# Kernel tuning notes

Measured on AMD Instinct MI355X. Metric: run time of the kernel, lower is better.

## Reference

```python
import jax, jax.numpy as jnp
import numpy as np

B, L, TOPK, NUM_RBF, NUM_POS, MAX_REL, CH = 4, 1024, 30, 16, 16, 32, 128
EDGE_IN = NUM_POS + NUM_RBF * 25 + 18  # 434
NODE_IN = 22


def _normalize(x, axis=-1):
    n = jnp.linalg.norm(x, axis=axis, keepdims=True)
    return jnp.where(n > 0, x / jnp.where(n > 0, n, 1.0), 0.0)


def layer_norm(x, g, b, eps=1e-5):
    mu = jnp.mean(x, axis=-1, keepdims=True)
    var = jnp.var(x, axis=-1, keepdims=True)
    return (x - mu) / jnp.sqrt(var + eps) * g + b


def gather_nodes_d(nodes, idx):
    # nodes [B,M,C], idx [B,N,K] -> [B,N,K,C]
    Bn, N, K = idx.shape
    out = jnp.take_along_axis(nodes, idx.reshape(Bn, N * K, 1), axis=1)
    return out.reshape(Bn, N, K, nodes.shape[-1])


def gather_edges(edges, idx):
    # edges [B,N,N,C], idx [B,N,K] -> [B,N,K,C]
    return jnp.take_along_axis(edges, idx[..., None], axis=2)


def cal_dihedral(Xf, eps=1e-7):
    U = _normalize(Xf[:, 1:, :] - Xf[:, :-1, :])
    u_0, u_1, u_2 = U[:, :-2], U[:, 1:-1], U[:, 2:]
    n_0 = _normalize(jnp.cross(u_0, u_1))
    n_1 = _normalize(jnp.cross(u_1, u_2))
    cosD = jnp.clip(jnp.sum(n_0 * n_1, -1), -1 + eps, 1 - eps)
    v = _normalize(jnp.cross(n_0, n_1))
    return jnp.sign(jnp.sum(-v * u_1, -1)) * jnp.arccos(cosD)


def _dihedrals(X, eps=1e-7):
    Bn, N = X.shape[0], X.shape[1]
    Xf = X[:, :, :3, :].reshape(Bn, 3 * N, 3)
    D = jnp.pad(cal_dihedral(Xf), ((0, 0), (1, 2))).reshape(Bn, N, 3)
    dihedral_feats = jnp.concatenate([jnp.cos(D), jnp.sin(D)], -1)
    U = _normalize(Xf[:, 1:, :] - Xf[:, :-1, :])
    cosA = jnp.clip(jnp.sum(U[:, :-2] * U[:, 1:-1], -1), -1 + eps, 1 - eps)
    A = jnp.pad(jnp.arccos(cosA), ((0, 0), (1, 2))).reshape(Bn, N, 3)
    angle_feats = jnp.concatenate([jnp.cos(A), jnp.sin(A)], -1)
    return jnp.concatenate([dihedral_feats, angle_feats], -1)  # [B,N,12]


def _quaternions(R):
    diag = jnp.diagonal(R, axis1=-2, axis2=-1)
    Rxx, Ryy, Rzz = diag[..., 0], diag[..., 1], diag[..., 2]
    mags = 0.5 * jnp.sqrt(jnp.abs(1.0 + jnp.stack([Rxx - Ryy - Rzz, -Rxx + Ryy - Rzz, -Rxx - Ryy + Rzz], -1)))
    signs = jnp.sign(jnp.stack([R[..., 2, 1] - R[..., 1, 2], R[..., 0, 2] - R[..., 2, 0], R[..., 1, 0] - R[..., 0, 1]], -1))
    w = jnp.sqrt(jax.nn.relu(1.0 + jnp.sum(diag, -1, keepdims=True))) / 2.0
    return _normalize(jnp.concatenate([signs * mags, w], -1))


def _orientations_coarse_gl_tuple(X, E_idx):
    V = X  # [B,N,4,3]
    Bn, N = X.shape[0], X.shape[1]
    Xf = X[:, :, :3, :].reshape(Bn, 3 * N, 3)
    U = _normalize(Xf[:, 1:, :] - Xf[:, :-1, :])
    u_0, u_1 = U[:, :-2], U[:, 1:-1]
    n_0 = _normalize(jnp.cross(u_0, u_1))[:, ::3]  # [B,N-1,3]
    b_1 = _normalize(u_0 - u_1)[:, ::3]
    Xa = Xf[:, ::3]  # N-atom coords [B,N,3]
    Q = jnp.stack([b_1, n_0, jnp.cross(b_1, n_0)], 2).reshape(Bn, N - 1, 9)
    Q = jnp.pad(Q, ((0, 0), (0, 1), (0, 0)))  # [B,N,9]
    Qm = Q.reshape(Bn, N, 3, 3)
    Q_neighbors = gather_nodes_d(Q, E_idx).reshape(Bn, N, -1, 3, 3)
    X_nb = gather_nodes_d(V[:, :, 1, :], E_idx)
    N_nb = gather_nodes_d(V[:, :, 0, :], E_idx)
    C_nb = gather_nodes_d(V[:, :, 2, :], E_idx)
    O_nb = gather_nodes_d(V[:, :, 3, :], E_idx)
    dXn = jnp.stack([X_nb, N_nb, C_nb, O_nb], 3) - Xa[:, :, None, None, :]  # [B,N,K,4,3]
    dU = jnp.einsum('bnij,bnkaj->bnkai', Qm, dXn)
    Kn = E_idx.shape[-1]
    E_direct = _normalize(dU).reshape(Bn, N, Kn, 12)
    R = jnp.einsum('bnji,bnkjl->bnkil', Qm, Q_neighbors)
    q = _quaternions(R)  # [B,N,K,4]
    dX_inner = V[:, :, jnp.array([0, 2, 3]), :] - Xa[:, :, None, :]
    V_direct = _normalize(jnp.einsum('bnij,bnaj->bnai', Qm, dX_inner)).reshape(Bn, N, 9)
    return V_direct, E_direct, q


def _dist(Xc, mask, eps=1e-6):
    mask_2D = mask[:, None, :] * mask[:, :, None]
    D = mask_2D * jnp.sqrt(jnp.sum((Xc[:, None, :, :] - Xc[:, :, None, :]) ** 2, -1) + eps)
    D_max = jnp.max(D, -1, keepdims=True)
    D_adjust = D + (1.0 - mask_2D) * D_max
    negD, E_idx = jax.lax.top_k(-D_adjust, min(TOPK, Xc.shape[1]))
    return -negD, E_idx


def _dist_seq(res_idx):
    D = jnp.abs(res_idx[:, :, None] - res_idx[:, None, :])
    _, E_idx = jax.lax.top_k(-D, min(TOPK, res_idx.shape[1]))
    return E_idx


def _rbf(D):
    D_mu = jnp.linspace(2.0, 22.0, NUM_RBF)
    D_sigma = (22.0 - 2.0) / NUM_RBF
    return jnp.exp(-(((D[..., None] - D_mu) / D_sigma) ** 2))


def _get_rbf(A, Bm, E_idx):
    D = jnp.sqrt(jnp.sum((A[:, :, None, :] - Bm[:, None, :, :]) ** 2, -1) + 1e-6)
    return _rbf(gather_edges(D[..., None], E_idx)[..., 0])


PAIRS = [('N', 'N'), ('C', 'C'), ('O', 'O'), ('Cb', 'Cb'), ('Ca', 'N'), ('Ca', 'C'), ('Ca', 'O'), ('Ca', 'Cb'),
         ('N', 'C'), ('N', 'O'), ('N', 'Cb'), ('Cb', 'C'), ('Cb', 'O'), ('O', 'C'), ('N', 'Ca'), ('C', 'Ca'),
         ('O', 'Ca'), ('Cb', 'Ca'), ('C', 'N'), ('O', 'N'), ('Cb', 'N'), ('C', 'Cb'), ('O', 'Cb'), ('C', 'O')]


def _forward(X, mask, residue_idx, chain_labels, W_pos, b_pos, W_edge, W_node, g_edge, b_edge, g_node, b_node):
    bvec = X[:, :, 1, :] - X[:, :, 0, :]
    cvec = X[:, :, 2, :] - X[:, :, 1, :]
    avec = jnp.cross(bvec, cvec)
    Cb = -0.58273431 * avec + 0.56802827 * bvec - 0.54067466 * cvec + X[:, :, 1, :]
    atoms = {'N': X[:, :, 0, :], 'Ca': X[:, :, 1, :], 'C': X[:, :, 2, :], 'O': X[:, :, 3, :], 'Cb': Cb}
    D_neighbors, E_idx = _dist(atoms['Ca'], mask)
    E_idx_res = _dist_seq(residue_idx)
    E_idx = jnp.where(mask[:, :, None] == 0, E_idx_res, E_idx)
    RBF_all = [_rbf(D_neighbors)]
    for pa, pb in PAIRS:
        RBF_all.append(_get_rbf(atoms[pa], atoms[pb], E_idx))
    RBF_all = jnp.concatenate(RBF_all, -1)  # [B,L,K,400]
    V_angles = _dihedrals(X) * mask[..., None]
    V_direct, E_direct, E_angles = _orientations_coarse_gl_tuple(X, E_idx)
    V_direct = V_direct * mask[..., None]
    offset = residue_idx[:, :, None] - residue_idx[:, None, :]
    E_offset = gather_edges(offset[..., None], E_idx)[..., 0]
    d_chains = (chain_labels[:, :, None] == chain_labels[:, None, :]).astype(jnp.int32)
    E_chains = gather_edges(d_chains[..., None], E_idx)[..., 0]
    d = jnp.clip(E_offset + MAX_REL, 0, 2 * MAX_REL) * E_chains + (1 - E_chains) * (2 * MAX_REL + 1)
    E_positional = jax.nn.one_hot(d, 2 * MAX_REL + 2, dtype=W_pos.dtype) @ W_pos + b_pos
    mask_j = gather_nodes_d(mask[..., None], E_idx)[..., 0]
    fdt = E_direct.dtype
    E = jnp.concatenate([E_positional, RBF_all, E_direct, E_angles,
                         E_chains[..., None].astype(fdt), mask_j[..., None]], -1)  # [B,L,K,434]
    E = layer_norm(E @ W_edge, g_edge, b_edge)
    Vn = jnp.concatenate([V_angles, V_direct, mask[..., None]], -1)  # [B,L,22]
    Vn = layer_norm(Vn @ W_node, g_node, b_node)
    return Vn, E, E_idx


def setup_inputs():
    key = jax.random.key(0)
    ks = jax.random.split(key, 8)
    X = 3.0 * jax.random.normal(ks[0], (B, L, 4, 3), jnp.float32)
    mask = jnp.ones((B, L), jnp.float32)
    residue_idx = jnp.tile(jnp.arange(L, dtype=jnp.int32), (B, 1))
    chain_labels = jax.random.randint(ks[1], (B, L), 0, 2, dtype=jnp.int32)
    s = lambda k, sh: jax.random.normal(k, sh, jnp.float32) * 0.05
    W_pos = s(ks[2], (2 * MAX_REL + 2, NUM_POS))
    b_pos = jnp.zeros((NUM_POS,), jnp.float32)
    W_edge = s(ks[3], (EDGE_IN, CH))
    W_node = s(ks[4], (NODE_IN, CH))
    return dict(X=X, mask=mask, residue_idx=residue_idx, chain_labels=chain_labels,
                W_pos=W_pos, b_pos=b_pos, W_edge=W_edge, W_node=W_node,
                g_edge=jnp.ones((CH,), jnp.float32), b_edge=jnp.zeros((CH,), jnp.float32),
                g_node=jnp.ones((CH,), jnp.float32), b_node=jnp.zeros((CH,), jnp.float32))


def reference(X, mask, residue_idx, chain_labels, W_pos, b_pos, W_edge, W_node, g_edge, b_edge, g_node, b_node):
    return _forward(X, mask, residue_idx, chain_labels, W_pos, b_pos, W_edge, W_node,
                    g_edge, b_edge, g_node, b_node)
```

## Files before the change

### kernel.cpp

```cpp
#include <hip/hip_runtime.h>

#define BATCH 4
#define LEN   1024
#define KNB   30
#define CH    128
#define EIN   434
#define KP    448
#define KST   14
#define ASTR  456
#define CSTR  132
#define AJS   20

typedef unsigned short ushort_t;
typedef __attribute__((ext_vector_type(8))) short bf16x8;
typedef __attribute__((ext_vector_type(4))) float f32x4;

__constant__ int c_pa[24] = {0,2,3,4,1,1,1,1,0,0,0,4,4,3,0,2,3,4,2,3,4,2,3,2};
__constant__ int c_pb[24] = {0,2,3,4,0,2,3,4,2,3,4,2,3,2,1,1,1,1,0,0,0,4,4,3};

struct F3 { float x, y, z; };
__device__ __forceinline__ F3 f3sub(F3 a, F3 b){ return {a.x-b.x, a.y-b.y, a.z-b.z}; }
__device__ __forceinline__ F3 f3cross(F3 a, F3 b){
  return {a.y*b.z - a.z*b.y, a.z*b.x - a.x*b.z, a.x*b.y - a.y*b.x};
}
__device__ __forceinline__ float f3dot(F3 a, F3 b){ return a.x*b.x + a.y*b.y + a.z*b.z; }
__device__ __forceinline__ F3 f3norm(F3 a){
  float s2 = f3dot(a,a);
  float inv = (s2 > 0.f) ? __builtin_amdgcn_rsqf(s2) : 0.f;
  return {a.x*inv, a.y*inv, a.z*inv};
}
__device__ __forceinline__ float fsign(float x){ return (x > 0.f) ? 1.f : ((x < 0.f) ? -1.f : 0.f); }
__device__ __forceinline__ float clip1(float c){ return fminf(fmaxf(c, -1.f + 1e-7f), 1.f - 1e-7f); }

__device__ __forceinline__ void dihedral_cs(F3 ua, F3 ub, F3 uc, float& c, float& s){
  F3 n0 = f3norm(f3cross(ua, ub));
  F3 n1 = f3norm(f3cross(ub, uc));
  float cd = clip1(f3dot(n0, n1));
  F3 v = f3norm(f3cross(n0, n1));
  c = cd;
  s = fsign(-f3dot(v, ub)) * sqrtf(1.f - cd*cd);
}

__device__ __forceinline__ ushort_t f2bf(float f){
  unsigned u = __float_as_uint(f);
  unsigned r = u + 0x7FFFu + ((u >> 16) & 1u);
  return (ushort_t)(r >> 16);
}

__device__ __forceinline__ unsigned cvt_pk(float a, float b){
  unsigned r;
  asm("v_cvt_pk_bf16_f32 %0, %1, %2" : "=v"(r) : "v"(a), "v"(b));
  return r;
}

#define DPP_MIN64_STEP(d, j, ctrl) do{                                        \
    unsigned td_ = (unsigned)__builtin_amdgcn_update_dpp(                     \
        (int)0xFFFFFFFF, (int)(d), (ctrl), 0xF, 0xF, false);                  \
    unsigned tj_ = (unsigned)__builtin_amdgcn_update_dpp(                     \
        (int)0xFFFFFFFF, (int)(j), (ctrl), 0xF, 0xF, false);                  \
    unsigned long long o_ = (((unsigned long long)td_) << 32) | tj_;          \
    unsigned long long c_ = (((unsigned long long)(d)) << 32) | (j);          \
    if (o_ < c_){ (d) = td_; (j) = tj_; }                                     \
  } while(0)
__device__ __forceinline__ void wave_min64(unsigned &d, unsigned &j){
  DPP_MIN64_STEP(d, j, 0x111);
  DPP_MIN64_STEP(d, j, 0x112);
  DPP_MIN64_STEP(d, j, 0x114);
  DPP_MIN64_STEP(d, j, 0x118);
  DPP_MIN64_STEP(d, j, 0x142);
  DPP_MIN64_STEP(d, j, 0x143);
  d = (unsigned)__builtin_amdgcn_readlane((int)d, 63);
  j = (unsigned)__builtin_amdgcn_readlane((int)j, 63);
}

__global__ __launch_bounds__(256) void prep_kernel(
    const float* __restrict__ X, const float* __restrict__ mask,
    const float* __restrict__ We,
    float* __restrict__ wCb, float* __restrict__ wQ, float* __restrict__ wVn,
    float* __restrict__ wCa, ushort_t* __restrict__ Wfrag)
{
  if (blockIdx.x >= 16){
    int f = (blockIdx.x - 16)*256 + threadIdx.x;
    if (f >= 8*KST*64) return;
    int t = f / (KST*64);
    int s = (f / 64) % KST;
    int l = f & 63;
    int n  = t*16 + (l & 15);
    int k0 = s*32 + (l >> 4)*8;
    ushort_t v[8];
    #pragma unroll
    for (int j = 0; j < 8; ++j){
      int k = k0 + j;
      v[j] = (k < EIN) ? f2bf(We[(size_t)k*CH + n]) : (ushort_t)0;
    }
    ulong2* dst = (ulong2*)(Wfrag + (size_t)f*8);
    *dst = *(ulong2*)v;
    return;
  }

  int idx = blockIdx.x * 256 + threadIdx.x;
  int n = idx & (LEN - 1);
  const float* p = X + (size_t)idx * 12;
  const float4* p4 = (const float4*)p;
  float4 q0 = p4[0], q1 = p4[1], q2 = p4[2];
  F3 Na = {q0.x, q0.y, q0.z};
  F3 Ca = {q0.w, q1.x, q1.y};
  F3 Cc = {q1.z, q1.w, q2.x};
  F3 Oa = {q2.y, q2.z, q2.w};
  ((float4*)wCa)[idx] = make_float4(Ca.x, Ca.y, Ca.z, 0.f);
  F3 bv = f3sub(Ca, Na);
  F3 cv = f3sub(Cc, Ca);
  F3 av = f3cross(bv, cv);
  ((float4*)wCb)[idx] = make_float4(
    -0.58273431f*av.x + 0.56802827f*bv.x - 0.54067466f*cv.x + Ca.x,
    -0.58273431f*av.y + 0.56802827f*bv.y - 0.54067466f*cv.y + Ca.y,
    -0.58273431f*av.z + 0.56802827f*bv.z - 0.54067466f*cv.z + Ca.z, 0.f);

  F3 u0 = f3norm(bv);
  F3 u1 = f3norm(cv);

  float Q[9];
  if (n < LEN - 1){
    F3 b1 = f3norm(f3sub(u0, u1));
    F3 n0 = f3norm(f3cross(u0, u1));
    F3 r2 = f3cross(b1, n0);
    Q[0]=b1.x; Q[1]=b1.y; Q[2]=b1.z;
    Q[3]=n0.x; Q[4]=n0.y; Q[5]=n0.z;
    Q[6]=r2.x; Q[7]=r2.y; Q[8]=r2.z;
  } else {
    #pragma unroll
    for (int t = 0; t < 9; ++t) Q[t] = 0.f;
  }
  float4* wq4 = (float4*)(wQ + (size_t)idx*12);
  wq4[0] = make_float4(Q[0], Q[1], Q[2], Q[3]);
  wq4[1] = make_float4(Q[4], Q[5], Q[6], Q[7]);
  wq4[2] = make_float4(Q[8], 0.f, 0.f, 0.f);

  float m = mask[idx];
  bool hp = (n > 0), hn = (n < LEN - 1);
  F3 um1 = {0,0,0}, u2 = {0,0,0}, u3 = {0,0,0};
  if (hp){
    const float* pp = p - 12;
    F3 Cp = {pp[6], pp[7], pp[8]};
    um1 = f3norm(f3sub(Na, Cp));
  }
  if (hn){
    const float* pn = p + 12;
    F3 Nn  = {pn[0], pn[1], pn[2]};
    F3 Can = {pn[3], pn[4], pn[5]};
    u2 = f3norm(f3sub(Nn, Cc));
    u3 = f3norm(f3sub(Can, Nn));
  }
  float cD0=1.f,sD0=0.f, cD1=1.f,sD1=0.f, cD2=1.f,sD2=0.f;
  float cA0=1.f,sA0=0.f, cA1=1.f,sA1=0.f, cA2=1.f,sA2=0.f;
  if (hp){
    dihedral_cs(um1, u0, u1, cD0, sD0);
    cA0 = clip1(f3dot(um1, u0)); sA0 = sqrtf(1.f - cA0*cA0);
  }
  if (hn){
    dihedral_cs(u0, u1, u2, cD1, sD1);
    dihedral_cs(u1, u2, u3, cD2, sD2);
    cA1 = clip1(f3dot(u0, u1)); sA1 = sqrtf(1.f - cA1*cA1);
    cA2 = clip1(f3dot(u1, u2)); sA2 = sqrtf(1.f - cA2*cA2);
  }
  float vn[22];
  vn[0] = cD0*m; vn[1] = cD1*m; vn[2]  = cD2*m;
  vn[3] = sD0*m; vn[4] = sD1*m; vn[5]  = sD2*m;
  vn[6] = cA0*m; vn[7] = cA1*m; vn[8]  = cA2*m;
  vn[9] = sA0*m; vn[10]= sA1*m; vn[11] = sA2*m;
  F3 dxs[3];
  dxs[0] = {0.f, 0.f, 0.f};
  dxs[1] = f3sub(Cc, Na);
  dxs[2] = f3sub(Oa, Na);
  #pragma unroll
  for (int a = 0; a < 3; ++a){
    F3 dv = dxs[a];
    F3 du = { Q[0]*dv.x + Q[1]*dv.y + Q[2]*dv.z,
              Q[3]*dv.x + Q[4]*dv.y + Q[5]*dv.z,
              Q[6]*dv.x + Q[7]*dv.y + Q[8]*dv.z };
    F3 dn = f3norm(du);
    vn[12 + a*3 + 0] = dn.x * m;
    vn[12 + a*3 + 1] = dn.y * m;
    vn[12 + a*3 + 2] = dn.z * m;
  }
  vn[21] = m;
  #pragma unroll
  for (int t = 0; t < 22; ++t) wVn[(size_t)idx*22 + t] = vn[t];
}

__global__ __launch_bounds__(256) void topk_kernel(
    const float* __restrict__ wCa, const float* __restrict__ wVn,
    const float* __restrict__ Wn,  const float* __restrict__ gn,
    const float* __restrict__ bn,
    float* __restrict__ wDn, int* __restrict__ wIdx,
    float* __restrict__ outI, float* __restrict__ outV)
{
  int wid = threadIdx.x >> 6, l = threadIdx.x & 63;
  int bi = blockIdx.x*4 + wid;
  int b  = bi >> 10;
  const float4* Ca = (const float4*)wCa;
  float4 ci = Ca[bi];
  const float4* Cb = Ca + (size_t)b * LEN;

  unsigned D[16];
  #pragma unroll
  for (int t = 0; t < 16; ++t){
    int j = l + 64*t;
    float4 cj = Cb[j];
    float dx = ci.x - cj.x, dy = ci.y - cj.y, dz = ci.z - cj.z;
    D[t] = __float_as_uint(sqrtf(dx*dx + dy*dy + dz*dz + 1e-6f));
  }
  unsigned lmin = D[0]; unsigned jmin = (unsigned)l;
  #pragma unroll
  for (int t = 1; t < 16; ++t)
    if (D[t] < lmin){ lmin = D[t]; jmin = (unsigned)(l + 64*t); }

  for (int k = 0; k < KNB; ++k){
    unsigned dmin = lmin, jw = jmin;
    wave_min64(dmin, jw);
    if (jmin == jw){
      wIdx[bi*KNB + k] = (int)jw;
      wDn[bi*KNB + k]  = __uint_as_float(dmin);
      outI[bi*KNB + k] = (float)jw;
      int tw = (int)(jw >> 6);
      #pragma unroll
      for (int t = 0; t < 16; ++t) if (t == tw) D[t] = 0xFFFFFFFFu;
      lmin = D[0]; jmin = (unsigned)l;
      #pragma unroll
      for (int t = 1; t < 16; ++t)
        if (D[t] < lmin){ lmin = D[t]; jmin = (unsigned)(l + 64*t); }
    }
  }

  float x0 = 0.f, x1 = 0.f;
  #pragma unroll
  for (int r = 0; r < 22; ++r){
    float vr = wVn[(size_t)bi*22 + r];
    x0 = fmaf(vr, Wn[r*CH + l],      x0);
    x1 = fmaf(vr, Wn[r*CH + l + 64], x1);
  }
  float sum = x0 + x1;
  #pragma unroll
  for (int off = 1; off < 64; off <<= 1) sum += __shfl_xor(sum, off);
  float mu = sum * (1.f/128.f);
  float d0 = x0 - mu, d1 = x1 - mu;
  float vs = d0*d0 + d1*d1;
  #pragma unroll
  for (int off = 1; off < 64; off <<= 1) vs += __shfl_xor(vs, off);
  float inv = 1.f / sqrtf(vs * (1.f/128.f) + 1e-5f);
  outV[(size_t)bi*CH + l]      = d0*inv*gn[l]    + bn[l];
  outV[(size_t)bi*CH + l + 64] = d1*inv*gn[l+64] + bn[l+64];
}

__global__ __launch_bounds__(256) void edge_kernel(
    const float* __restrict__ X, const float* __restrict__ mask,
    const int* __restrict__ resi, const int* __restrict__ chain,
    const float* __restrict__ Wp, const float* __restrict__ bp,
    const float* __restrict__ ge, const float* __restrict__ be,
    const float* __restrict__ wCb, const float* __restrict__ wQ,
    const float* __restrict__ wDn, const int* __restrict__ wIdx,
    const ushort_t* __restrict__ Wfrag,
    float* __restrict__ outE)
{
  __shared__ __align__(16) ushort_t As[32*ASTR];
  __shared__ __align__(16) float sAJ[KNB][AJS];
  __shared__ __align__(16) float sAI[16];
  __shared__ __align__(16) float sQi[12];

  int bi  = blockIdx.x;
  int b   = bi >> 10;
  int tid = threadIdx.x;
  int w   = tid >> 6, l = tid & 63;

  float qj0=0.f,qj1=0.f,qj2=0.f,qj3=0.f,qj4=0.f,qj5=0.f,qj6=0.f,qj7=0.f,qj8=0.f;
  if (w == 0 && l < KNB){
    int j  = wIdx[bi*KNB + l];
    int gj = (b << 10) + j;
    const float4* pj4 = (const float4*)(X + (size_t)gj * 12);
    *(float4*)&sAJ[l][0] = pj4[0];
    *(float4*)&sAJ[l][4] = pj4[1];
    *(float4*)&sAJ[l][8] = pj4[2];
  } else if (w == 1 && l < KNB){
    int j  = wIdx[bi*KNB + l];
    int gj = (b << 10) + j;
    *(float4*)&sAJ[l][12] = ((const float4*)wCb)[gj];
    sAJ[l][15] = wDn[bi*KNB + l];
    sAJ[l][16] = (chain[bi] == chain[gj]) ? 1.f : 0.f;
    sAJ[l][17] = mask[gj];
    sAJ[l][18] = (float)(resi[bi] - resi[gj]);
  } else if (w == 2 && l >= KNB && l < 2*KNB){
    int k  = l - KNB;
    int j  = wIdx[bi*KNB + k];
    int gj = (b << 10) + j;
    const float4* q4 = (const float4*)(wQ + (size_t)gj * 12);
    float4 a = q4[0], bq = q4[1], cq = q4[2];
    qj0=a.x; qj1=a.y; qj2=a.z; qj3=a.w;
    qj4=bq.x; qj5=bq.y; qj6=bq.z; qj7=bq.w;
    qj8=cq.x;
  } else if (w == 3 && l == 0){
    const float4* pi4 = (const float4*)(X + (size_t)bi * 12);
    *(float4*)&sAI[0]  = pi4[0];
    *(float4*)&sAI[4]  = pi4[1];
    *(float4*)&sAI[8]  = pi4[2];
    *(float4*)&sAI[12] = ((const float4*)wCb)[bi];
  } else if (w == 3 && l == 1){
    const float4* q4 = (const float4*)(wQ + (size_t)bi * 12);
    *(float4*)&sQi[0] = q4[0];
    *(float4*)&sQi[4] = q4[1];
    *(float4*)&sQi[8] = q4[2];
  }
  for (int e = tid; e < KNB*14; e += 256){
    int r = e / 14, c = EIN + (e % 14);
    As[r*ASTR + c] = 0;
  }
  __syncthreads();

  auto rbf_task = [&](int tau){
    int k = (int)(((unsigned)tau * 5243u) >> 17);
    int p = tau - k*25;
    float d;
    if (p == 0) d = sAJ[k][15];
    else {
      int ai = c_pa[p-1]*3, bj = c_pb[p-1]*3;
      float dx = sAI[ai+0] - sAJ[k][bj+0];
      float dy = sAI[ai+1] - sAJ[k][bj+1];
      float dz = sAI[ai+2] - sAJ[k][bj+2];
      d = sqrtf(dx*dx + dy*dy + dz*dz + 1e-6f);
    }
    float A  = d*d*(-0.92332483f);
    float Bc = d*1.84664966f;
    ushort_t* dst = &As[k*ASTR + 16 + p*16];
    unsigned u[8];
    #pragma unroll
    for (int h = 0; h < 8; ++h){
      float mu0 = 2.f + (2*h  )*(4.f/3.f);
      float mu1 = 2.f + (2*h+1)*(4.f/3.f);
      float e0 = __builtin_amdgcn_exp2f(fmaf(Bc, mu0, A + (-0.92332483f*mu0*mu0)));
      float e1 = __builtin_amdgcn_exp2f(fmaf(Bc, mu1, A + (-0.92332483f*mu1*mu1)));
      u[h] = cvt_pk(e0, e1);
    }
    *(uint4*)&dst[0] = make_uint4(u[0], u[1], u[2], u[3]);
    *(uint4*)&dst[8] = make_uint4(u[4], u[5], u[6], u[7]);
  };

  if (w == 0){
    rbf_task(l); rbf_task(l+64); rbf_task(l+128); rbf_task(l+192);
  } else if (w == 1){
    rbf_task(256+l); rbf_task(320+l); rbf_task(384+l);
    if (l < KNB){
      int k = l;
      ushort_t* row = &As[k*ASTR];
      float ch = sAJ[k][16];
      int off  = (int)sAJ[k][18];
      int dpos = off + 32;
      dpos = dpos < 0 ? 0 : (dpos > 64 ? 64 : dpos);
      if (!(ch > 0.5f)) dpos = 65;
      const float4* wp4 = (const float4*)(Wp + dpos*16);
      const float4* bp4 = (const float4*)bp;
      unsigned u[8];
      #pragma unroll
      for (int h = 0; h < 4; ++h){
        float4 wv = wp4[h], bv = bp4[h];
        u[2*h]   = cvt_pk(wv.x + bv.x, wv.y + bv.y);
        u[2*h+1] = cvt_pk(wv.z + bv.z, wv.w + bv.w);
      }
      *(uint4*)&row[0] = make_uint4(u[0], u[1], u[2], u[3]);
      *(uint4*)&row[8] = make_uint4(u[4], u[5], u[6], u[7]);
      *(unsigned*)&row[432] = cvt_pk(ch, sAJ[k][17]);
    }
  } else if (w == 2){
    rbf_task(448+l); rbf_task(512+l);
    if (l >= KNB && l < 2*KNB){
      int k = l - KNB;
      ushort_t* row = &As[k*ASTR];
      float R[3][3];
      R[0][0] = sQi[0]*qj0 + sQi[3]*qj3 + sQi[6]*qj6;
      R[0][1] = sQi[0]*qj1 + sQi[3]*qj4 + sQi[6]*qj7;
      R[0][2] = sQi[0]*qj2 + sQi[3]*qj5 + sQi[6]*qj8;
      R[1][0] = sQi[1]*qj0 + sQi[4]*qj3 + sQi[7]*qj6;
      R[1][1] = sQi[1]*qj1 + sQi[4]*qj4 + sQi[7]*qj7;
      R[1][2] = sQi[1]*qj2 + sQi[4]*qj5 + sQi[7]*qj8;
      R[2][0] = sQi[2]*qj0 + sQi[5]*qj3 + sQi[8]*qj6;
      R[2][1] = sQi[2]*qj1 + sQi[5]*qj4 + sQi[8]*qj7;
      R[2][2] = sQi[2]*qj2 + sQi[5]*qj5 + sQi[8]*qj8;
      float Rxx = R[0][0], Ryy = R[1][1], Rzz = R[2][2];
      float mx = 0.5f*sqrtf(fabsf(1.f + Rxx - Ryy - Rzz));
      float my = 0.5f*sqrtf(fabsf(1.f - Rxx + Ryy - Rzz));
      float mz = 0.5f*sqrtf(fabsf(1.f - Rxx - Ryy + Rzz));
      float qx = fsign(R[2][1] - R[1][2]) * mx;
      float qy = fsign(R[0][2] - R[2][0]) * my;
      float qz = fsign(R[1][0] - R[0][1]) * mz;
      float qw = sqrtf(fmaxf(1.f + Rxx + Ryy + Rzz, 0.f)) * 0.5f;
      float qn2 = qx*qx + qy*qy + qz*qz + qw*qw;
      float inv = qn2 > 0.f ? __builtin_amdgcn_rsqf(qn2) : 0.f;
      *(uint2*)&row[428] = make_uint2(cvt_pk(qx*inv, qy*inv), cvt_pk(qz*inv, qw*inv));
    }
  } else {
    rbf_task(576+l); rbf_task(640+l);
    { int t2 = 704+l; if (t2 < 750) rbf_task(t2); }
    if (l < KNB){
      int k = l;
      ushort_t* row = &As[k*ASTR];
      float nx = sAI[0], ny = sAI[1], nz = sAI[2];
      const int amap[4] = {3, 0, 6, 9};
      float f[12];
      #pragma unroll
      for (int a = 0; a < 4; ++a){
        float dx = sAJ[k][amap[a]+0] - nx;
        float dy = sAJ[k][amap[a]+1] - ny;
        float dz = sAJ[k][amap[a]+2] - nz;
        float e0 = sQi[0]*dx + sQi[1]*dy + sQi[2]*dz;
        float e1 = sQi[3]*dx + sQi[4]*dy + sQi[5]*dz;
        float e2 = sQi[6]*dx + sQi[7]*dy + sQi[8]*dz;
        float ss = e0*e0 + e1*e1 + e2*e2;
        float inv = ss > 0.f ? __builtin_amdgcn_rsqf(ss) : 0.f;
        f[a*3+0] = e0*inv; f[a*3+1] = e1*inv; f[a*3+2] = e2*inv;
      }
      unsigned u[6];
      #pragma unroll
      for (int h = 0; h < 6; ++h) u[h] = cvt_pk(f[2*h], f[2*h+1]);
      *(uint4*)&row[416] = make_uint4(u[0], u[1], u[2], u[3]);
      *(uint2*)&row[424] = make_uint2(u[4], u[5]);
    }
  }
  __syncthreads();

  int n0 = w*2;
  int aOff0 = (l & 15)*ASTR + (l >> 4)*8;
  int aOff1 = aOff0 + 16*ASTR;
  const ushort_t* bpw0 = Wfrag + ((size_t)(n0    *KST)*64 + l)*8;
  const ushort_t* bpw1 = Wfrag + ((size_t)((n0+1)*KST)*64 + l)*8;

  f32x4 acc00 = {0.f,0.f,0.f,0.f}, acc01 = acc00, acc10 = acc00, acc11 = acc00;

  bf16x8 a0 = *(const bf16x8*)&As[aOff0];
  bf16x8 a1 = *(const bf16x8*)&As[aOff1];
  bf16x8 b0 = *(const bf16x8*)bpw0;
  bf16x8 b1 = *(const bf16x8*)bpw1;
  #pragma unroll
  for (int s = 0; s < KST; ++s){
    bf16x8 a0n, a1n, b0n, b1n;
    if (s < KST-1){
      int ka = (s+1)*32;
      a0n = *(const bf16x8*)&As[aOff0 + ka];
      a1n = *(const bf16x8*)&As[aOff1 + ka];
      b0n = *(const bf16x8*)(bpw0 + (size_t)(s+1)*64*8);
      b1n = *(const bf16x8*)(bpw1 + (size_t)(s+1)*64*8);
    }
    acc00 = __builtin_amdgcn_mfma_f32_16x16x32_bf16(a0, b0, acc00, 0, 0, 0);
    acc01 = __builtin_amdgcn_mfma_f32_16x16x32_bf16(a0, b1, acc01, 0, 0, 0);
    acc10 = __builtin_amdgcn_mfma_f32_16x16x32_bf16(a1, b0, acc10, 0, 0, 0);
    acc11 = __builtin_amdgcn_mfma_f32_16x16x32_bf16(a1, b1, acc11, 0, 0, 0);
    if (s < KST-1){ a0 = a0n; a1 = a1n; b0 = b0n; b1 = b1n; }
  }
  __syncthreads();

  float* Cs = (float*)As;
  int ccol = l & 15, crow = (l >> 4)*4;
  #pragma unroll
  for (int r = 0; r < 4; ++r){
    Cs[(crow + r)*CSTR      + n0*16 + ccol]      = acc00[r];
    Cs[(crow + r)*CSTR      + (n0+1)*16 + ccol]  = acc01[r];
    Cs[(16 + crow + r)*CSTR + n0*16 + ccol]      = acc10[r];
    Cs[(16 + crow + r)*CSTR + (n0+1)*16 + ccol]  = acc11[r];
  }
  __syncthreads();

  if (tid < KNB*8){
    int row = tid >> 3, g = tid & 7;
    const float4* vr = (const float4*)&Cs[row*CSTR + g*16];
    float4 v0 = vr[0], v1 = vr[1], v2 = vr[2], v3 = vr[3];
    float v[16] = {v0.x,v0.y,v0.z,v0.w, v1.x,v1.y,v1.z,v1.w,
                   v2.x,v2.y,v2.z,v2.w, v3.x,v3.y,v3.z,v3.w};
    float s = 0.f;
    #pragma unroll
    for (int c = 0; c < 16; ++c) s += v[c];
    #pragma unroll
    for (int off = 1; off < 8; off <<= 1) s += __shfl_xor(s, off, 8);
    float mu = s * (1.f/128.f);
    float vs = 0.f;
    #pragma unroll
    for (int c = 0; c < 16; ++c){ float dd = v[c] - mu; vs += dd*dd; }
    #pragma unroll
    for (int off = 1; off < 8; off <<= 1) vs += __shfl_xor(vs, off, 8);
    float inv = 1.f / sqrtf(vs * (1.f/128.f) + 1e-5f);
    float o[16];
    #pragma unroll
    for (int c = 0; c < 16; ++c)
      o[c] = (v[c] - mu)*inv*ge[g*16 + c] + be[g*16 + c];
    float4* dst = (float4*)&outE[((size_t)bi*KNB + row)*CH + g*16];
    dst[0] = make_float4(o[0], o[1], o[2], o[3]);
    dst[1] = make_float4(o[4], o[5], o[6], o[7]);
    dst[2] = make_float4(o[8], o[9], o[10], o[11]);
    dst[3] = make_float4(o[12], o[13], o[14], o[15]);
  }
}

extern "C" void kernel_launch(void* const* d_in, const int* in_sizes, int n_in,
                              void* d_out, int out_size, void* d_ws, size_t ws_size,
                              hipStream_t stream)
{
  const float* X    = (const float*)d_in[0];
  const float* mask = (const float*)d_in[1];
  const int*   resi = (const int*)  d_in[2];
  const int*   chn  = (const int*)  d_in[3];
  const float* Wp   = (const float*)d_in[4];
  const float* bp   = (const float*)d_in[5];
  const float* We   = (const float*)d_in[6];
  const float* Wn   = (const float*)d_in[7];
  const float* ge   = (const float*)d_in[8];
  const float* be   = (const float*)d_in[9];
  const float* gn   = (const float*)d_in[10];
  const float* bn   = (const float*)d_in[11];

  float* outV = (float*)d_out;
  float* outE = outV + (size_t)BATCH*LEN*CH;
  float* outI = outE + (size_t)BATCH*LEN*KNB*CH;

  float* ws   = (float*)d_ws;
  float* wCb  = ws;
  float* wQ   = wCb + (size_t)BATCH*LEN*4;
  float* wVn  = wQ  + (size_t)BATCH*LEN*12;
  float* wDn  = wVn + (size_t)BATCH*LEN*22;
  int*   wIdx = (int*)(wDn + (size_t)BATCH*LEN*KNB);
  float* wCa  = (float*)(wIdx + (size_t)BATCH*LEN*KNB);
  ushort_t* Wfrag = (ushort_t*)(wCa + (size_t)BATCH*LEN*4);

  prep_kernel<<<16 + 28, 256, 0, stream>>>(X, mask, We, wCb, wQ, wVn, wCa, Wfrag);
  topk_kernel<<<BATCH*LEN/4, 256, 0, stream>>>(wCa, wVn, Wn, gn, bn,
                                               wDn, wIdx, outI, outV);
  edge_kernel<<<BATCH*LEN, 256, 0, stream>>>(X, mask, resi, chn, Wp, bp, ge, be,
                                             wCb, wQ, wDn, wIdx, Wfrag, outE);
}
```

Measured before the change: 171.8 us.

## Double edge kernel block to 512 threads and permute RBF column layout

The edge kernel now runs with 512 threads, so each wave handles one 16-column MFMA tile instead of two. RBF tasks are spread evenly over all threads rather than assigned per wave. The RBF columns are split into low and high halves of 8 values each, so each task writes two contiguous 16-byte chunks, and the weight-fragment prep permutes rows to match. The LayerNorm epilogue also uses 16 threads per row. This adds parallelism and latency hiding, at the cost of larger blocks that may lower occupancy and less reuse of the A fragments per wave.

```diff
diff --git a/kernel.cpp b/kernel.cpp
--- a/kernel.cpp
+++ b/kernel.cpp
@@ -51,6 +51,13 @@
   unsigned r;
   asm("v_cvt_pk_bf16_f32 %0, %1, %2" : "=v"(r) : "v"(a), "v"(b));
   return r;
+}
+
+__device__ __forceinline__ int corig(int c){
+  if (c < 16 || c >= 416) return c;
+  int base = (c < 216) ? 16 : 216;
+  int p = (c - base) >> 3, m = (c - base) & 7;
+  return 16 + p*16 + m + ((c < 216) ? 0 : 8);
 }
 
 #define DPP_MIN64_STEP(d, j, ctrl) do{                                        \
@@ -91,7 +98,7 @@
     #pragma unroll
     for (int j = 0; j < 8; ++j){
       int k = k0 + j;
-      v[j] = (k < EIN) ? f2bf(We[(size_t)k*CH + n]) : (ushort_t)0;
+      v[j] = (k < EIN) ? f2bf(We[(size_t)corig(k)*CH + n]) : (ushort_t)0;
     }
     ulong2* dst = (ulong2*)(Wfrag + (size_t)f*8);
     *dst = *(ulong2*)v;
@@ -252,7 +259,7 @@
   outV[(size_t)bi*CH + l + 64] = d1*inv*gn[l+64] + bn[l+64];
 }
 
-__global__ __launch_bounds__(256) void edge_kernel(
+__global__ __launch_bounds__(512) void edge_kernel(
     const float* __restrict__ X, const float* __restrict__ mask,
     const int* __restrict__ resi, const int* __restrict__ chain,
     const float* __restrict__ Wp, const float* __restrict__ bp,
@@ -288,9 +295,8 @@
     sAJ[l][16] = (chain[bi] == chain[gj]) ? 1.f : 0.f;
     sAJ[l][17] = mask[gj];
     sAJ[l][18] = (float)(resi[bi] - resi[gj]);
-  } else if (w == 2 && l >= KNB && l < 2*KNB){
-    int k  = l - KNB;
-    int j  = wIdx[bi*KNB + k];
+  } else if (w == 2 && l < KNB){
+    int j  = wIdx[bi*KNB + l];
     int gj = (b << 10) + j;
     const float4* q4 = (const float4*)(wQ + (size_t)gj * 12);
     float4 a = q4[0], bq = q4[1], cq = q4[2];
@@ -309,7 +315,7 @@
     *(float4*)&sQi[4] = q4[1];
     *(float4*)&sQi[8] = q4[2];
   }
-  for (int e = tid; e < KNB*14; e += 256){
+  for (int e = tid; e < KNB*14; e += 512){
     int r = e / 14, c = EIN + (e % 14);
     As[r*ASTR + c] = 0;
   }
@@ -329,7 +335,6 @@
     }
     float A  = d*d*(-0.92332483f);
     float Bc = d*1.84664966f;
-    ushort_t* dst = &As[k*ASTR + 16 + p*16];
     unsigned u[8];
     #pragma unroll
     for (int h = 0; h < 8; ++h){
@@ -339,119 +344,104 @@
       float e1 = __builtin_amdgcn_exp2f(fmaf(Bc, mu1, A + (-0.92332483f*mu1*mu1)));
       u[h] = cvt_pk(e0, e1);
     }
-    *(uint4*)&dst[0] = make_uint4(u[0], u[1], u[2], u[3]);
-    *(uint4*)&dst[8] = make_uint4(u[4], u[5], u[6], u[7]);
+    *(uint4*)&As[k*ASTR + 16  + p*8] = make_uint4(u[0], u[1], u[2], u[3]);
+    *(uint4*)&As[k*ASTR + 216 + p*8] = make_uint4(u[4], u[5], u[6], u[7]);
   };
 
-  if (w == 0){
-    rbf_task(l); rbf_task(l+64); rbf_task(l+128); rbf_task(l+192);
-  } else if (w == 1){
-    rbf_task(256+l); rbf_task(320+l); rbf_task(384+l);
-    if (l < KNB){
-      int k = l;
-      ushort_t* row = &As[k*ASTR];
-      float ch = sAJ[k][16];
-      int off  = (int)sAJ[k][18];
-      int dpos = off + 32;
-      dpos = dpos < 0 ? 0 : (dpos > 64 ? 64 : dpos);
-      if (!(ch > 0.5f)) dpos = 65;
-      const float4* wp4 = (const float4*)(Wp + dpos*16);
-      const float4* bp4 = (const float4*)bp;
-      unsigned u[8];
-      #pragma unroll
-      for (int h = 0; h < 4; ++h){
-        float4 wv = wp4[h], bv = bp4[h];
-        u[2*h]   = cvt_pk(wv.x + bv.x, wv.y + bv.y);
-        u[2*h+1] = cvt_pk(wv.z + bv.z, wv.w + bv.w);
-      }
-      *(uint4*)&row[0] = make_uint4(u[0], u[1], u[2], u[3]);
-      *(uint4*)&row[8] = make_uint4(u[4], u[5], u[6], u[7]);
-      *(unsigned*)&row[432] = cvt_pk(ch, sAJ[k][17]);
-    }
-  } else if (w == 2){
-    rbf_task(448+l); rbf_task(512+l);
-    if (l >= KNB && l < 2*KNB){
-      int k = l - KNB;
-      ushort_t* row = &As[k*ASTR];
-      float R[3][3];
-      R[0][0] = sQi[0]*qj0 + sQi[3]*qj3 + sQi[6]*qj6;
-      R[0][1] = sQi[0]*qj1 + sQi[3]*qj4 + sQi[6]*qj7;
-      R[0][2] = sQi[0]*qj2 + sQi[3]*qj5 + sQi[6]*qj8;
-      R[1][0] = sQi[1]*qj0 + sQi[4]*qj3 + sQi[7]*qj6;
-      R[1][1] = sQi[1]*qj1 + sQi[4]*qj4 + sQi[7]*qj7;
-      R[1][2] = sQi[1]*qj2 + sQi[4]*qj5 + sQi[7]*qj8;
-      R[2][0] = sQi[2]*qj0 + sQi[5]*qj3 + sQi[8]*qj6;
-      R[2][1] = sQi[2]*qj1 + sQi[5]*qj4 + sQi[8]*qj7;
-      R[2][2] = sQi[2]*qj2 + sQi[5]*qj5 + sQi[8]*qj8;
-      float Rxx = R[0][0], Ryy = R[1][1], Rzz = R[2][2];
-      float mx = 0.5f*sqrtf(fabsf(1.f + Rxx - Ryy - Rzz));
-      float my = 0.5f*sqrtf(fabsf(1.f - Rxx + Ryy - Rzz));
-      float mz = 0.5f*sqrtf(fabsf(1.f - Rxx - Ryy + Rzz));
-      float qx = fsign(R[2][1] - R[1][2]) * mx;
-      float qy = fsign(R[0][2] - R[2][0]) * my;
-      float qz = fsign(R[1][0] - R[0][1]) * mz;
-      float qw = sqrtf(fmaxf(1.f + Rxx + Ryy + Rzz, 0.f)) * 0.5f;
-      float qn2 = qx*qx + qy*qy + qz*qz + qw*qw;
-      float inv = qn2 > 0.f ? __builtin_amdgcn_rsqf(qn2) : 0.f;
-      *(uint2*)&row[428] = make_uint2(cvt_pk(qx*inv, qy*inv), cvt_pk(qz*inv, qw*inv));
-    }
-  } else {
-    rbf_task(576+l); rbf_task(640+l);
-    { int t2 = 704+l; if (t2 < 750) rbf_task(t2); }
-    if (l < KNB){
-      int k = l;
-      ushort_t* row = &As[k*ASTR];
-      float nx = sAI[0], ny = sAI[1], nz = sAI[2];
-      const int amap[4] = {3, 0, 6, 9};
-      float f[12];
-      #pragma unroll
-      for (int a = 0; a < 4; ++a){
-        float dx = sAJ[k][amap[a]+0] - nx;
-        float dy = sAJ[k][amap[a]+1] - ny;
-        float dz = sAJ[k][amap[a]+2] - nz;
-        float e0 = sQi[0]*dx + sQi[1]*dy + sQi[2]*dz;
-        float e1 = sQi[3]*dx + sQi[4]*dy + sQi[5]*dz;
-        float e2 = sQi[6]*dx + sQi[7]*dy + sQi[8]*dz;
-        float ss = e0*e0 + e1*e1 + e2*e2;
-        float inv = ss > 0.f ? __builtin_amdgcn_rsqf(ss) : 0.f;
-        f[a*3+0] = e0*inv; f[a*3+1] = e1*inv; f[a*3+2] = e2*inv;
-      }
-      unsigned u[6];
-      #pragma unroll
-      for (int h = 0; h < 6; ++h) u[h] = cvt_pk(f[2*h], f[2*h+1]);
-      *(uint4*)&row[416] = make_uint4(u[0], u[1], u[2], u[3]);
-      *(uint2*)&row[424] = make_uint2(u[4], u[5]);
-    }
+  rbf_task(tid);
+  if (tid >= 274) rbf_task(tid + 238);
+
+  if (w == 1 && l < KNB){
+    int k = l;
+    ushort_t* row = &As[k*ASTR];
+    float ch = sAJ[k][16];
+    int off  = (int)sAJ[k][18];
+    int dpos = off + 32;
+    dpos = dpos < 0 ? 0 : (dpos > 64 ? 64 : dpos);
+    if (!(ch > 0.5f)) dpos = 65;
+    const float4* wp4 = (const float4*)(Wp + dpos*16);
+    const float4* bp4 = (const float4*)bp;
+    unsigned u[8];
+    #pragma unroll
+    for (int h = 0; h < 4; ++h){
+      float4 wv = wp4[h], bv = bp4[h];
+      u[2*h]   = cvt_pk(wv.x + bv.x, wv.y + bv.y);
+      u[2*h+1] = cvt_pk(wv.z + bv.z, wv.w + bv.w);
+    }
+    *(uint4*)&row[0] = make_uint4(u[0], u[1], u[2], u[3]);
+    *(uint4*)&row[8] = make_uint4(u[4], u[5], u[6], u[7]);
+    *(unsigned*)&row[432] = cvt_pk(ch, sAJ[k][17]);
+  } else if (w == 2 && l < KNB){
+    int k = l;
+    ushort_t* row = &As[k*ASTR];
+    float R[3][3];
+    R[0][0] = sQi[0]*qj0 + sQi[3]*qj3 + sQi[6]*qj6;
+    R[0][1] = sQi[0]*qj1 + sQi[3]*qj4 + sQi[6]*qj7;
+    R[0][2] = sQi[0]*qj2 + sQi[3]*qj5 + sQi[6]*qj8;
+    R[1][0] = sQi[1]*qj0 + sQi[4]*qj3 + sQi[7]*qj6;
+    R[1][1] = sQi[1]*qj1 + sQi[4]*qj4 + sQi[7]*qj7;
+    R[1][2] = sQi[1]*qj2 + sQi[4]*qj5 + sQi[7]*qj8;
+    R[2][0] = sQi[2]*qj0 + sQi[5]*qj3 + sQi[8]*qj6;
+    R[2][1] = sQi[2]*qj1 + sQi[5]*qj4 + sQi[8]*qj7;
+    R[2][2] = sQi[2]*qj2 + sQi[5]*qj5 + sQi[8]*qj8;
+    float Rxx = R[0][0], Ryy = R[1][1], Rzz = R[2][2];
+    float mx = 0.5f*sqrtf(fabsf(1.f + Rxx - Ryy - Rzz));
+    float my = 0.5f*sqrtf(fabsf(1.f - Rxx + Ryy - Rzz));
+    float mz = 0.5f*sqrtf(fabsf(1.f - Rxx - Ryy + Rzz));
+    float qx = fsign(R[2][1] - R[1][2]) * mx;
+    float qy = fsign(R[0][2] - R[2][0]) * my;
+    float qz = fsign(R[1][0] - R[0][1]) * mz;
+    float qw = sqrtf(fmaxf(1.f + Rxx + Ryy + Rzz, 0.f)) * 0.5f;
+    float qn2 = qx*qx + qy*qy + qz*qz + qw*qw;
+    float inv = qn2 > 0.f ? __builtin_amdgcn_rsqf(qn2) : 0.f;
+    *(uint2*)&row[428] = make_uint2(cvt_pk(qx*inv, qy*inv), cvt_pk(qz*inv, qw*inv));
+  } else if (w == 3 && l < KNB){
+    int k = l;
+    ushort_t* row = &As[k*ASTR];
+    float nx = sAI[0], ny = sAI[1], nz = sAI[2];
+    const int amap[4] = {3, 0, 6, 9};
+    float f[12];
+    #pragma unroll
+    for (int a = 0; a < 4; ++a){
+      float dx = sAJ[k][amap[a]+0] - nx;
+      float dy = sAJ[k][amap[a]+1] - ny;
+      float dz = sAJ[k][amap[a]+2] - nz;
+      float e0 = sQi[0]*dx + sQi[1]*dy + sQi[2]*dz;
+      float e1 = sQi[3]*dx + sQi[4]*dy + sQi[5]*dz;
+      float e2 = sQi[6]*dx + sQi[7]*dy + sQi[8]*dz;
+      float ss = e0*e0 + e1*e1 + e2*e2;
+      float inv = ss > 0.f ? __builtin_amdgcn_rsqf(ss) : 0.f;
+      f[a*3+0] = e0*inv; f[a*3+1] = e1*inv; f[a*3+2] = e2*inv;
+    }
+    unsigned u[6];
+    #pragma unroll
+    for (int h = 0; h < 6; ++h) u[h] = cvt_pk(f[2*h], f[2*h+1]);
+    *(uint4*)&row[416] = make_uint4(u[0], u[1], u[2], u[3]);
+    *(uint2*)&row[424] = make_uint2(u[4], u[5]);
   }
   __syncthreads();
 
-  int n0 = w*2;
   int aOff0 = (l & 15)*ASTR + (l >> 4)*8;
   int aOff1 = aOff0 + 16*ASTR;
-  const ushort_t* bpw0 = Wfrag + ((size_t)(n0    *KST)*64 + l)*8;
-  const ushort_t* bpw1 = Wfrag + ((size_t)((n0+1)*KST)*64 + l)*8;
-
-  f32x4 acc00 = {0.f,0.f,0.f,0.f}, acc01 = acc00, acc10 = acc00, acc11 = acc00;
+  const ushort_t* bpw = Wfrag + ((size_t)(w*KST)*64 + l)*8;
+
+  f32x4 acc0 = {0.f,0.f,0.f,0.f}, acc1 = acc0;
 
   bf16x8 a0 = *(const bf16x8*)&As[aOff0];
   bf16x8 a1 = *(const bf16x8*)&As[aOff1];
-  bf16x8 b0 = *(const bf16x8*)bpw0;
-  bf16x8 b1 = *(const bf16x8*)bpw1;
+  bf16x8 b0 = *(const bf16x8*)bpw;
   #pragma unroll
   for (int s = 0; s < KST; ++s){
-    bf16x8 a0n, a1n, b0n, b1n;
+    bf16x8 a0n, a1n, b0n;
     if (s < KST-1){
       int ka = (s+1)*32;
       a0n = *(const bf16x8*)&As[aOff0 + ka];
       a1n = *(const bf16x8*)&As[aOff1 + ka];
-      b0n = *(const bf16x8*)(bpw0 + (size_t)(s+1)*64*8);
-      b1n = *(const bf16x8*)(bpw1 + (size_t)(s+1)*64*8);
-    }
-    acc00 = __builtin_amdgcn_mfma_f32_16x16x32_bf16(a0, b0, acc00, 0, 0, 0);
-    acc01 = __builtin_amdgcn_mfma_f32_16x16x32_bf16(a0, b1, acc01, 0, 0, 0);
-    acc10 = __builtin_amdgcn_mfma_f32_16x16x32_bf16(a1, b0, acc10, 0, 0, 0);
-    acc11 = __builtin_amdgcn_mfma_f32_16x16x32_bf16(a1, b1, acc11, 0, 0, 0);
-    if (s < KST-1){ a0 = a0n; a1 = a1n; b0 = b0n; b1 = b1n; }
+      b0n = *(const bf16x8*)(bpw + (size_t)(s+1)*64*8);
+    }
+    acc0 = __builtin_amdgcn_mfma_f32_16x16x32_bf16(a0, b0, acc0, 0, 0, 0);
+    acc1 = __builtin_amdgcn_mfma_f32_16x16x32_bf16(a1, b0, acc1, 0, 0, 0);
+    if (s < KST-1){ a0 = a0n; a1 = a1n; b0 = b0n; }
   }
   __syncthreads();
 
@@ -459,40 +449,39 @@
   int ccol = l & 15, crow = (l >> 4)*4;
   #pragma unroll
   for (int r = 0; r < 4; ++r){
-    Cs[(crow + r)*CSTR      + n0*16 + ccol]      = acc00[r];
-    Cs[(crow + r)*CSTR      + (n0+1)*16 + ccol]  = acc01[r];
-    Cs[(16 + crow + r)*CSTR + n0*16 + ccol]      = acc10[r];
-    Cs[(16 + crow + r)*CSTR + (n0+1)*16 + ccol]  = acc11[r];
+    Cs[(crow + r)*CSTR      + w*16 + ccol] = acc0[r];
+    Cs[(16 + crow + r)*CSTR + w*16 + ccol] = acc1[r];
   }
   __syncthreads();
 
-  if (tid < KNB*8){
-    int row = tid >> 3, g = tid & 7;
-    const float4* vr = (const float4*)&Cs[row*CSTR + g*16];
-    float4 v0 = vr[0], v1 = vr[1], v2 = vr[2], v3 = vr[3];
-    float v[16] = {v0.x,v0.y,v0.z,v0.w, v1.x,v1.y,v1.z,v1.w,
-                   v2.x,v2.y,v2.z,v2.w, v3.x,v3.y,v3.z,v3.w};
+  if (tid < KNB*16){
+    int row = tid >> 4, g = tid & 15;
+    const float4* vr = (const float4*)&Cs[row*CSTR + g*8];
+    float4 v0 = vr[0], v1 = vr[1];
+    float v[8] = {v0.x,v0.y,v0.z,v0.w, v1.x,v1.y,v1.z,v1.w};
     float s = 0.f;
     #pragma unroll
-    for (int c = 0; c < 16; ++c) s += v[c];
-    #pragma unroll
-    for (int off = 1; off < 8; off <<= 1) s += __shfl_xor(s, off, 8);
+    for (int c = 0; c < 8; ++c) s += v[c];
+    #pragma unroll
+    for (int off = 1; off < 16; off <<= 1) s += __shfl_xor(s, off, 16);
     float mu = s * (1.f/128.f);
     float vs = 0.f;
     #pragma unroll
-    for (int c = 0; c < 16; ++c){ float dd = v[c] - mu; vs += dd*dd; }
-    #pragma unroll
-    for (int off = 1; off < 8; off <<= 1) vs += __shfl_xor(vs, off, 8);
+    for (int c = 0; c < 8; ++c){ float dd = v[c] - mu; vs += dd*dd; }
+    #pragma unroll
+    for (int off = 1; off < 16; off <<= 1) vs += __shfl_xor(vs, off, 16);
     float inv = 1.f / sqrtf(vs * (1.f/128.f) + 1e-5f);
-    float o[16];
-    #pragma unroll
-    for (int c = 0; c < 16; ++c)
-      o[c] = (v[c] - mu)*inv*ge[g*16 + c] + be[g*16 + c];
-    float4* dst = (float4*)&outE[((size_t)bi*KNB + row)*CH + g*16];
-    dst[0] = make_float4(o[0], o[1], o[2], o[3]);
-    dst[1] = make_float4(o[4], o[5], o[6], o[7]);
-    dst[2] = make_float4(o[8], o[9], o[10], o[11]);
-    dst[3] = make_float4(o[12], o[13], o[14], o[15]);
+    const float4* g4 = (const float4*)&ge[g*8];
+    const float4* b4 = (const float4*)&be[g*8];
+    float4 ga = g4[0], gb = g4[1], ba = b4[0], bb = b4[1];
+    float4 o0, o1;
+    o0.x = (v[0]-mu)*inv*ga.x + ba.x;  o0.y = (v[1]-mu)*inv*ga.y + ba.y;
+    o0.z = (v[2]-mu)*inv*ga.z + ba.z;  o0.w = (v[3]-mu)*inv*ga.w + ba.w;
+    o1.x = (v[4]-mu)*inv*gb.x + bb.x;  o1.y = (v[5]-mu)*inv*gb.y + bb.y;
+    o1.z = (v[6]-mu)*inv*gb.z + bb.z;  o1.w = (v[7]-mu)*inv*gb.w + bb.w;
+    float4* dst = (float4*)&outE[((size_t)bi*KNB + row)*CH + g*8];
+    dst[0] = o0;
+    dst[1] = o1;
   }
 }
 
@@ -529,6 +518,6 @@
   prep_kernel<<<16 + 28, 256, 0, stream>>>(X, mask, We, wCb, wQ, wVn, wCa, Wfrag);
   topk_kernel<<<BATCH*LEN/4, 256, 0, stream>>>(wCa, wVn, Wn, gn, bn,
                                                wDn, wIdx, outI, outV);
-  edge_kernel<<<BATCH*LEN, 256, 0, stream>>>(X, mask, resi, chn, Wp, bp, ge, be,
+  edge_kernel<<<BATCH*LEN, 512, 0, stream>>>(X, mask, resi, chn, Wp, bp, ge, be,
                                              wCb, wQ, wDn, wIdx, Wfrag, outE);
 }
```

New measurement: 161.0 us. -6.3%, faster.
